# Kernel tuning notes

Measured on AMD Instinct MI355X. Metric: run time of the kernel, lower is better.

Reference implementation:

```python
import jax, jax.numpy as jnp
import numpy as np

E = 8
HIDDEN = 1024
INTER = 4096
CAPS = np.array([512, 1024, 2048, 4096, 1024, 512, 2048, 1024], dtype=np.int64)  # sum = 12288
TOTAL = int(CAPS.sum())


def setup_inputs() -> dict:
    key = jax.random.key(0)
    k1, k2, k3, k4, k5 = jax.random.split(key, 5)
    s1 = 1.0 / np.sqrt(HIDDEN)
    s2 = 1.0 / np.sqrt(INTER)
    return {
        "inter_state": jax.random.normal(k1, (TOTAL, HIDDEN), dtype=jnp.float32),
        "w1": jax.random.normal(k2, (E, INTER, HIDDEN), dtype=jnp.float32) * s1,
        "b1": jax.random.normal(k3, (E, INTER), dtype=jnp.float32) * s1,
        "w2": jax.random.normal(k4, (E, HIDDEN, INTER), dtype=jnp.float32) * s2,
        "b2": jax.random.normal(k5, (E, HIDDEN), dtype=jnp.float32) * s2,
        "capacities": jnp.asarray(CAPS),
    }


def reference(inter_state, w1, b1, w2, b2, capacities):
    # Grouped GEMM: tokens are contiguous per expert with sizes = capacities.
    # Capacities are routing metadata (static for slicing).
    caps = np.asarray(capacities)
    offs = np.concatenate([[0], np.cumsum(caps)]).astype(np.int64)
    outs = []
    for e in range(caps.shape[0]):  # small fixed expert loop
        x = inter_state[int(offs[e]):int(offs[e + 1])]      # [cap_e, hidden]
        h = x @ w1[e].T + b1[e]                              # [cap_e, inter]
        outs.append(h @ w2[e].T + b2[e])                     # [cap_e, hidden]
    return jnp.concatenate(outs, axis=0)                     # [total, hidden]
```

## Files before the change

kernel.cpp:

```cpp
#include <hip/hip_runtime.h>
#include <hip/hip_bf16.h>

#define DEV __device__ __forceinline__

typedef __bf16 bf16x8 __attribute__((ext_vector_type(8)));
typedef float  f32x4  __attribute__((ext_vector_type(4)));


DEV unsigned short f2bf(float f) {
  union { float f; unsigned u; } v; v.f = f;
  unsigned u = v.u;
  return (unsigned short)((u + 0x7FFFu + ((u >> 16) & 1u)) >> 16);
}

DEV float bf2f(unsigned short s) {
  union { unsigned u; float f; } v; v.u = (unsigned)s << 16; return v.f;
}

DEV void gld_lds16(const void* g, void* l) {
  __builtin_amdgcn_global_load_lds(
      (const __attribute__((address_space(1))) unsigned int*)g,
      (__attribute__((address_space(3))) unsigned int*)l, 16, 0, 0);
}

#define WAITVM(N) asm volatile("s_waitcnt vmcnt(" #N ")" ::: "memory"); \
                  __builtin_amdgcn_sched_barrier(0)
#define WAITLG(N) asm volatile("s_waitcnt lgkmcnt(" #N ")" ::: "memory"); \
                  __builtin_amdgcn_sched_barrier(0)
#define BARRIER() __builtin_amdgcn_s_barrier(); __builtin_amdgcn_sched_barrier(0)

template <int KT_, int KLEN, int SK, int N_, int NCT, bool OUT_BF16,
          bool HAS_BIAS, int EDIV>
__global__ __launch_bounds__(512, 2)
void gemm256p(const unsigned short* __restrict__ A,
              const unsigned short* __restrict__ B,
              const float* __restrict__ bias,
              void* __restrict__ C0, void* __restrict__ C1) {
  __shared__ __align__(128) char lds[131072];
  constexpr int NT = KLEN / 64;

  const int tid  = threadIdx.x;
  const int lane = tid & 63;
  const int wv   = tid >> 6;
  const int wm   = wv >> 2;
  const int wn   = wv & 3;
  const int fr   = lane & 15;
  const int fq   = lane >> 4;

  int bid = blockIdx.x;
  const int nwg = gridDim.x;
  bid = (bid & 7) * (nwg >> 3) + (bid >> 3);

  int sk = 0;
  if constexpr (SK > 1) {
    const int per = nwg / SK;
    sk = bid / per;
    bid -= sk * per;
  }
  const int kStart = sk * KLEN;
  void* Cv = (SK > 1 && sk == 1) ? C1 : C0;

  const int rt = bid / NCT;
  const int ct = bid - rt * NCT;

  int e;
  if constexpr (EDIV > 0) {
    e = rt / EDIV;
  } else {
    const int cums[9] = {0, 2, 6, 14, 30, 34, 36, 44, 48};
    e = 0;
#pragma unroll
    for (int i = 1; i < 8; ++i) e += (rt >= cums[i]) ? 1 : 0;
  }

  const int grow0 = rt * 256;
  const int nloc0 = ct * 256;
  const unsigned short* Bg = B + (size_t)e * N_ * KT_;

  f32x4 acc[8][4];
#pragma unroll
  for (int i = 0; i < 8; ++i)
#pragma unroll
    for (int j = 0; j < 4; ++j) acc[i][j] = (f32x4){0.f, 0.f, 0.f, 0.f};

  auto stage_half = [&](int t, int h) {
    const int kb = kStart + t * 64;
    char* dst = lds + (h >> 1) * 65536 + (t & 1) * 32768 + (h & 1) * 16384;
    const unsigned short* src = (h < 2) ? A : Bg;
    const int row0 = (h < 2) ? (grow0 + (h & 1) * 128) : (nloc0 + (h & 1) * 128);
#pragma unroll
    for (int s = 0; s < 2; ++s) {
      int o  = s * 8192 + wv * 1024 + lane * 16;
      int r  = o >> 7;
      int cb = (o & 127) ^ ((r & 7) << 4);
      gld_lds16(src + (size_t)(row0 + r) * KT_ + kb + (cb >> 1),
                dst + s * 8192 + wv * 1024);
    }
  };

  stage_half(0, 0); stage_half(0, 1); stage_half(0, 2); stage_half(0, 3);
  if constexpr (NT > 1) { stage_half(1, 2); stage_half(1, 3); }

  const int brow0 = (wn & 1) * 64;

  for (int t = 0; t < NT; ++t) {
    char* Ah = lds + (t & 1) * 32768 + wm * 16384;
    char* Bh = lds + 65536 + (t & 1) * 32768 + ((wn >> 1) * 16384);

    if (t + 1 < NT) { WAITVM(4); } else { WAITVM(0); }
    BARRIER();

    bf16x8 bfr[4][2], afX[2][2], afY[2][2];
#pragma unroll
    for (int ni = 0; ni < 4; ++ni) {
      int r = brow0 + ni * 16 + fr;
#pragma unroll
      for (int k = 0; k < 2; ++k)
        bfr[ni][k] = *(bf16x8*)(Bh + r * 128 + ((k * 64 + fq * 16) ^ ((r & 7) << 4)));
    }
#pragma unroll
    for (int j = 0; j < 2; ++j) {
      int r = j * 16 + fr;
#pragma unroll
      for (int k = 0; k < 2; ++k)
        afX[j][k] = *(bf16x8*)(Ah + r * 128 + ((k * 64 + fq * 16) ^ ((r & 7) << 4)));
    }
#pragma unroll
    for (int j = 0; j < 2; ++j) {
      int r = 32 + j * 16 + fr;
#pragma unroll
      for (int k = 0; k < 2; ++k)
        afY[j][k] = *(bf16x8*)(Ah + r * 128 + ((k * 64 + fq * 16) ^ ((r & 7) << 4)));
    }
    if (t + 1 < NT) stage_half(t + 1, 0);
    WAITLG(4);
    BARRIER();
    __builtin_amdgcn_s_setprio(1);
#pragma unroll
    for (int k = 0; k < 2; ++k)
#pragma unroll
      for (int j = 0; j < 2; ++j)
#pragma unroll
        for (int ni = 0; ni < 4; ++ni)
          acc[j][ni] = __builtin_amdgcn_mfma_f32_16x16x32_bf16(
              afX[j][k], bfr[ni][k], acc[j][ni], 0, 0, 0);
    __builtin_amdgcn_s_setprio(0);
#pragma unroll
    for (int j = 0; j < 2; ++j) {
      int r = 64 + j * 16 + fr;
#pragma unroll
      for (int k = 0; k < 2; ++k)
        afX[j][k] = *(bf16x8*)(Ah + r * 128 + ((k * 64 + fq * 16) ^ ((r & 7) << 4)));
    }
    if (t + 1 < NT) stage_half(t + 1, 1);
    if (t + 2 < NT) stage_half(t + 2, 2);
    WAITLG(4);
    __builtin_amdgcn_s_setprio(1);
#pragma unroll
    for (int k = 0; k < 2; ++k)
#pragma unroll
      for (int j = 0; j < 2; ++j)
#pragma unroll
        for (int ni = 0; ni < 4; ++ni)
          acc[2 + j][ni] = __builtin_amdgcn_mfma_f32_16x16x32_bf16(
              afY[j][k], bfr[ni][k], acc[2 + j][ni], 0, 0, 0);
    __builtin_amdgcn_s_setprio(0);
#pragma unroll
    for (int j = 0; j < 2; ++j) {
      int r = 96 + j * 16 + fr;
#pragma unroll
      for (int k = 0; k < 2; ++k)
        afY[j][k] = *(bf16x8*)(Ah + r * 128 + ((k * 64 + fq * 16) ^ ((r & 7) << 4)));
    }
    if (t + 2 < NT) stage_half(t + 2, 3);
    WAITLG(4);
    __builtin_amdgcn_s_setprio(1);
#pragma unroll
    for (int k = 0; k < 2; ++k)
#pragma unroll
      for (int j = 0; j < 2; ++j)
#pragma unroll
        for (int ni = 0; ni < 4; ++ni)
          acc[4 + j][ni] = __builtin_amdgcn_mfma_f32_16x16x32_bf16(
              afX[j][k], bfr[ni][k], acc[4 + j][ni], 0, 0, 0);
    __builtin_amdgcn_s_setprio(0);
    WAITLG(0);
    __builtin_amdgcn_s_setprio(1);
#pragma unroll
    for (int k = 0; k < 2; ++k)
#pragma unroll
      for (int j = 0; j < 2; ++j)
#pragma unroll
        for (int ni = 0; ni < 4; ++ni)
          acc[6 + j][ni] = __builtin_amdgcn_mfma_f32_16x16x32_bf16(
              afY[j][k], bfr[ni][k], acc[6 + j][ni], 0, 0, 0);
    __builtin_amdgcn_s_setprio(0);
  }

#pragma unroll
  for (int ni = 0; ni < 4; ++ni) {
    int ncol = nloc0 + wn * 64 + ni * 16 + fr;
    float bv = 0.f;
    if constexpr (HAS_BIAS) bv = (bias + (size_t)e * N_)[ncol];
#pragma unroll
    for (int mi = 0; mi < 8; ++mi) {
      int m = grow0 + wm * 128 + mi * 16 + fq * 4;
#pragma unroll
      for (int j = 0; j < 4; ++j) {
        float val = acc[mi][ni][j] + bv;
        if constexpr (OUT_BF16)
          ((unsigned short*)Cv)[(size_t)(m + j) * N_ + ncol] = f2bf(val);
        else
          ((float*)Cv)[(size_t)(m + j) * N_ + ncol] = val;
      }
    }
  }
}

template <int K_, int N_, int NCT, bool OUT_BF16, bool HAS_BIAS, int EDIV>
__global__ __launch_bounds__(256, 2)
void gemm128(const unsigned short* __restrict__ A,
             const unsigned short* __restrict__ B,
             const float* __restrict__ bias, void* __restrict__ Cv) {
  __shared__ __align__(128) char lds[2][32768];
  constexpr int NT = K_ / 64;

  const int tid  = threadIdx.x;
  const int lane = tid & 63;
  const int wv   = tid >> 6;
  const int wm   = wv >> 1;
  const int wn   = wv & 1;
  const int fr   = lane & 15;
  const int fq   = lane >> 4;

  int bid = blockIdx.x;
  const int nwg = gridDim.x;
  bid = (bid & 7) * (nwg >> 3) + (bid >> 3);

  const int rt = bid / NCT;
  const int ct = bid - rt * NCT;

  int e;
  if constexpr (EDIV > 0) {
    e = rt / EDIV;
  } else {
    const int cums[9] = {0, 4, 12, 28, 60, 68, 72, 88, 96};
    e = 0;
#pragma unroll
    for (int i = 1; i < 8; ++i) e += (rt >= cums[i]) ? 1 : 0;
  }

  const int grow0 = rt * 128;
  const int nloc0 = ct * 128;
  const unsigned short* Bg = B + (size_t)e * N_ * K_;

  f32x4 acc[4][4];
#pragma unroll
  for (int i = 0; i < 4; ++i)
#pragma unroll
    for (int j = 0; j < 4; ++j) acc[i][j] = (f32x4){0.f, 0.f, 0.f, 0.f};

  auto stage = [&](int buf, int tk) {
    const int kb = tk * 64;
#pragma unroll
    for (int s = 0; s < 4; ++s) {
      int o  = s * 4096 + wv * 1024 + lane * 16;
      int r  = o >> 7;
      int cb = (o & 127) ^ ((r & 7) << 4);
      gld_lds16(A + (size_t)(grow0 + r) * K_ + kb + (cb >> 1),
                lds[buf] + s * 4096 + wv * 1024);
    }
#pragma unroll
    for (int s = 0; s < 4; ++s) {
      int o  = s * 4096 + wv * 1024 + lane * 16;
      int r  = o >> 7;
      int cb = (o & 127) ^ ((r & 7) << 4);
      gld_lds16(Bg + (size_t)(nloc0 + r) * K_ + kb + (cb >> 1),
                lds[buf] + 16384 + s * 4096 + wv * 1024);
    }
  };

  stage(0, 0);
  for (int t = 0; t < NT; ++t) {
    const int cur = t & 1;
    if (t + 1 < NT) {
      stage(cur ^ 1, t + 1);
      WAITVM(8);
    } else {
      WAITVM(0);
    }
    BARRIER();

    char* Ab = lds[cur];
    char* Bb = lds[cur] + 16384;
    bf16x8 af[4][2], bf[4][2];
#pragma unroll
    for (int mi = 0; mi < 4; ++mi) {
      int r = wm * 64 + mi * 16 + fr;
#pragma unroll
      for (int k = 0; k < 2; ++k)
        af[mi][k] = *(bf16x8*)(Ab + r * 128 + ((k * 64 + fq * 16) ^ ((r & 7) << 4)));
    }
#pragma unroll
    for (int ni = 0; ni < 4; ++ni) {
      int r = wn * 64 + ni * 16 + fr;
#pragma unroll
      for (int k = 0; k < 2; ++k)
        bf[ni][k] = *(bf16x8*)(Bb + r * 128 + ((k * 64 + fq * 16) ^ ((r & 7) << 4)));
    }
    WAITLG(0);
    __builtin_amdgcn_s_setprio(1);
#pragma unroll
    for (int k = 0; k < 2; ++k)
#pragma unroll
      for (int mi = 0; mi < 4; ++mi)
#pragma unroll
        for (int ni = 0; ni < 4; ++ni)
          acc[mi][ni] = __builtin_amdgcn_mfma_f32_16x16x32_bf16(
              af[mi][k], bf[ni][k], acc[mi][ni], 0, 0, 0);
    __builtin_amdgcn_s_setprio(0);
    BARRIER();
  }

#pragma unroll
  for (int ni = 0; ni < 4; ++ni) {
    int ncol = nloc0 + wn * 64 + ni * 16 + fr;
    float bv = 0.f;
    if constexpr (HAS_BIAS) bv = (bias + (size_t)e * N_)[ncol];
#pragma unroll
    for (int mi = 0; mi < 4; ++mi) {
      int m = grow0 + wm * 64 + mi * 16 + fq * 4;
#pragma unroll
      for (int j = 0; j < 4; ++j) {
        float val = acc[mi][ni][j] + bv;
        if constexpr (OUT_BF16)
          ((unsigned short*)Cv)[(size_t)(m + j) * N_ + ncol] = f2bf(val);
        else
          ((float*)Cv)[(size_t)(m + j) * N_ + ncol] = val;
      }
    }
  }
}

__global__ __launch_bounds__(256)
void reduce_bf16(const unsigned short* __restrict__ p0,
                 const unsigned short* __restrict__ p1,
                 unsigned short* __restrict__ out, int n8) {
  for (int i = blockIdx.x * 256 + threadIdx.x; i < n8; i += gridDim.x * 256) {
    ushort4 a0 = ((const ushort4*)p0)[2 * i];
    ushort4 a1 = ((const ushort4*)p0)[2 * i + 1];
    ushort4 b0 = ((const ushort4*)p1)[2 * i];
    ushort4 b1 = ((const ushort4*)p1)[2 * i + 1];
    ushort4 r0 = {f2bf(bf2f(a0.x) + bf2f(b0.x)), f2bf(bf2f(a0.y) + bf2f(b0.y)),
                  f2bf(bf2f(a0.z) + bf2f(b0.z)), f2bf(bf2f(a0.w) + bf2f(b0.w))};
    ushort4 r1 = {f2bf(bf2f(a1.x) + bf2f(b1.x)), f2bf(bf2f(a1.y) + bf2f(b1.y)),
                  f2bf(bf2f(a1.z) + bf2f(b1.z)), f2bf(bf2f(a1.w) + bf2f(b1.w))};
    ((ushort4*)out)[2 * i]     = r0;
    ((ushort4*)out)[2 * i + 1] = r1;
  }
}

DEV int swz(int r, int cbyte) {
  return (r * 64 + cbyte) ^ (((r >> 1) & 7) << 4);
}

template <int K_, int N_, bool OUT_BF16, bool HAS_BIAS, int EDIV>
__global__ __launch_bounds__(512, 2)
void gemm8(const unsigned short* __restrict__ A,
           const unsigned short* __restrict__ B,
           const float* __restrict__ bias, void* __restrict__ Cv) {
  __shared__ __align__(128) char lds[2][49152];
  const int t    = threadIdx.x;
  const int lane = t & 63;
  const int wv   = t >> 6;
  const int wm   = wv >> 1;
  const int wn   = wv & 1;
  const int fr   = lane & 15;
  const int fq   = lane >> 4;
  constexpr int NCT = N_ / 128;
  constexpr int NT  = K_ / 64;

  int bid = blockIdx.x;
  const int nwg = gridDim.x;
  bid = (bid & 7) * (nwg >> 3) + (bid >> 3);
  const int rt = bid / NCT;
  const int ct = bid - rt * NCT;

  int e;
  if constexpr (EDIV > 0) {
    e = rt / EDIV;
  } else {
    const int cums[9] = {0, 2, 6, 14, 30, 34, 36, 44, 48};
    e = 0;
#pragma unroll
    for (int i = 1; i < 8; ++i) e += (rt >= cums[i]) ? 1 : 0;
  }

  const int grow0 = rt * 256;
  const int nloc0 = ct * 128;
  const unsigned short* Bg = B + (size_t)e * N_ * K_;

  f32x4 acc[4][4];
#pragma unroll
  for (int i = 0; i < 4; ++i)
#pragma unroll
    for (int j = 0; j < 4; ++j) acc[i][j] = (f32x4){0.f, 0.f, 0.f, 0.f};

  auto stage = [&](int buf, int tk) {
    const int kb = tk * 64;
    char* Abase = lds[buf];
    char* Bbase = lds[buf] + 32768;
#pragma unroll
    for (int s = 0; s < 4; ++s) {
      int o  = s * 8192 + wv * 1024 + lane * 16;
      int r  = o >> 7;
      int cb = (o & 127) ^ ((r & 7) << 4);
      gld_lds16(A + (size_t)(grow0 + r) * K_ + kb + (cb >> 1),
                Abase + s * 8192 + wv * 1024);
    }
#pragma unroll
    for (int s = 0; s < 2; ++s) {
      int o  = s * 8192 + wv * 1024 + lane * 16;
      int r  = o >> 7;
      int cb = (o & 127) ^ ((r & 7) << 4);
      gld_lds16(Bg + (size_t)(nloc0 + r) * K_ + kb + (cb >> 1),
                Bbase + s * 8192 + wv * 1024);
    }
  };

  auto compute = [&](int buf) {
    char* Abase = lds[buf];
    char* Bbase = lds[buf] + 32768;
    bf16x8 af[4][2], bf[4][2];
#pragma unroll
    for (int mi = 0; mi < 4; ++mi) {
      int r = wm * 64 + mi * 16 + fr;
#pragma unroll
      for (int k = 0; k < 2; ++k)
        af[mi][k] = *(bf16x8*)(Abase + r * 128 + ((k * 64 + fq * 16) ^ ((r & 7) << 4)));
    }
#pragma unroll
    for (int ni = 0; ni < 4; ++ni) {
      int r = wn * 64 + ni * 16 + fr;
#pragma unroll
      for (int k = 0; k < 2; ++k)
        bf[ni][k] = *(bf16x8*)(Bbase + r * 128 + ((k * 64 + fq * 16) ^ ((r & 7) << 4)));
    }
    __builtin_amdgcn_s_setprio(1);
#pragma unroll
    for (int k = 0; k < 2; ++k)
#pragma unroll
      for (int mi = 0; mi < 4; ++mi)
#pragma unroll
        for (int ni = 0; ni < 4; ++ni)
          acc[mi][ni] = __builtin_amdgcn_mfma_f32_16x16x32_bf16(
              af[mi][k], bf[ni][k], acc[mi][ni], 0, 0, 0);
    __builtin_amdgcn_s_setprio(0);
  };

  stage(0, 0);
  for (int tk = 0; tk < NT; ++tk) {
    const int cur = tk & 1;
    if (tk + 1 < NT) {
      stage(cur ^ 1, tk + 1);
      WAITVM(6);
    } else {
      WAITVM(0);
    }
    __builtin_amdgcn_s_barrier();
    compute(cur);
    WAITLG(0);
    __builtin_amdgcn_s_barrier();
  }

#pragma unroll
  for (int ni = 0; ni < 4; ++ni) {
    int nloc = nloc0 + wn * 64 + ni * 16 + fr;
    float bv = 0.f;
    if constexpr (HAS_BIAS) bv = (bias + (size_t)e * N_)[nloc];
#pragma unroll
    for (int mi = 0; mi < 4; ++mi) {
      int m = grow0 + wm * 64 + mi * 16 + fq * 4;
#pragma unroll
      for (int j = 0; j < 4; ++j) {
        float val = acc[mi][ni][j] + bv;
        if constexpr (OUT_BF16)
          ((unsigned short*)Cv)[(size_t)(m + j) * N_ + nloc] = f2bf(val);
        else
          ((float*)Cv)[(size_t)(m + j) * N_ + nloc] = val;
      }
    }
  }
}

template <int K_, int N_, int NCT_, bool OUT_BF16, bool HAS_BIAS, int EDIV>
__global__ __launch_bounds__(256)
void gemm_expert(const void* __restrict__ Av, const void* __restrict__ Bv,
                 const float* __restrict__ bias, void* __restrict__ Cv) {
  __shared__ char lds[2][12288];
  const int t    = threadIdx.x;
  const int lane = t & 63;
  const int wv   = t >> 6;
  const int wr   = wv >> 1;
  const int wc   = wv & 1;
  const int fr   = lane & 15;
  const int fq   = lane >> 4;

  int bid = blockIdx.x;
  const int nwg = gridDim.x;
  if ((nwg & 7) == 0) bid = (bid & 7) * (nwg >> 3) + (bid >> 3);
  const int rt = bid / NCT_;
  const int ct = bid - rt * NCT_;

  int e;
  if constexpr (EDIV > 0) {
    e = rt / EDIV;
  } else {
    const int cums[9] = {0, 4, 12, 28, 60, 68, 72, 88, 96};
    e = 0;
#pragma unroll
    for (int i = 1; i < 8; ++i) e += (rt >= cums[i]) ? 1 : 0;
  }

  const int grow0 = rt * 128;
  const int nloc0 = ct * 64;

  f32x4 acc[4][2];
#pragma unroll
  for (int i = 0; i < 4; ++i)
#pragma unroll
    for (int j = 0; j < 2; ++j) acc[i][j] = (f32x4){0.f, 0.f, 0.f, 0.f};

  const float* Af = (const float*)Av;
  const unsigned short* Bb = (const unsigned short*)Bv + (size_t)e * N_ * K_;

  auto stage = [&](int buf, int kb) {
    char* As = lds[buf];
    char* Bs = lds[buf] + 8192;
#pragma unroll
    for (int it = 0; it < 4; ++it) {
      int q = t + it * 256, r = q >> 3, c = (q & 7) * 4;
      float4 f = *(const float4*)(Af + (size_t)(grow0 + r) * K_ + kb + c);
      ushort4 v = {f2bf(f.x), f2bf(f.y), f2bf(f.z), f2bf(f.w)};
      *(ushort4*)(As + swz(r, c * 2)) = v;
    }
    int o = wv * 1024 + lane * 16;
    int p = o ^ (((o >> 7) & 7) << 4);
    gld_lds16(Bb + (size_t)(nloc0 + (p >> 6)) * K_ + kb + ((p & 63) >> 1),
              Bs + wv * 1024);
  };

  auto compute = [&](int buf) {
    char* As = lds[buf];
    char* Bs = lds[buf] + 8192;
    bf16x8 af[4], bfg[2];
#pragma unroll
    for (int mi = 0; mi < 4; ++mi)
      af[mi] = *(bf16x8*)(As + swz(wr * 64 + mi * 16 + fr, fq * 16));
#pragma unroll
    for (int ni = 0; ni < 2; ++ni)
      bfg[ni] = *(bf16x8*)(Bs + swz(wc * 32 + ni * 16 + fr, fq * 16));
#pragma unroll
    for (int mi = 0; mi < 4; ++mi)
#pragma unroll
      for (int ni = 0; ni < 2; ++ni)
        acc[mi][ni] = __builtin_amdgcn_mfma_f32_16x16x32_bf16(
            af[mi], bfg[ni], acc[mi][ni], 0, 0, 0);
  };

  int cur = 0;
  stage(0, 0);
  __syncthreads();
  for (int kb = 32; kb < K_; kb += 32) {
    stage(cur ^ 1, kb);
    compute(cur);
    __syncthreads();
    cur ^= 1;
  }
  compute(cur);

#pragma unroll
  for (int ni = 0; ni < 2; ++ni) {
    int nloc = nloc0 + wc * 32 + ni * 16 + fr;
    float bv = 0.f;
    if constexpr (HAS_BIAS) bv = (bias + (size_t)e * N_)[nloc];
#pragma unroll
    for (int mi = 0; mi < 4; ++mi) {
      int m = grow0 + wr * 64 + mi * 16 + fq * 4;
#pragma unroll
      for (int j = 0; j < 4; ++j) {
        float val = acc[mi][ni][j] + bv;
        if constexpr (OUT_BF16)
          ((unsigned short*)Cv)[(size_t)(m + j) * N_ + nloc] = f2bf(val);
        else
          ((float*)Cv)[(size_t)(m + j) * N_ + nloc] = val;
      }
    }
  }
}

__global__ __launch_bounds__(256)
void transpose_w1(const float* __restrict__ w1, unsigned short* __restrict__ w1t) {
  __shared__ unsigned short tl[64 * 68];
  int b = blockIdx.x;
  int jt = b & 15, kt = (b >> 4) & 63, e = b >> 10;
  const float* src = w1 + ((size_t)e * 4096 + kt * 64) * 1024 + jt * 64;
  int t = threadIdx.x;
#pragma unroll
  for (int it = 0; it < 4; ++it) {
    int q = t + it * 256, kr = q >> 4, jc = (q & 15) * 4;
    float4 f = *(const float4*)(src + (size_t)kr * 1024 + jc);
    ushort4 v = {f2bf(f.x), f2bf(f.y), f2bf(f.z), f2bf(f.w)};
    *(ushort4*)&tl[kr * 68 + jc] = v;
  }
  __syncthreads();
  unsigned short* dst = w1t + ((size_t)e * 1024 + jt * 64) * 4096 + kt * 64;
#pragma unroll
  for (int it = 0; it < 4; ++it) {
    int q = t + it * 256, jr = q >> 4, kc = (q & 15) * 4;
    ushort4 v = {tl[(kc + 0) * 68 + jr], tl[(kc + 1) * 68 + jr],
                 tl[(kc + 2) * 68 + jr], tl[(kc + 3) * 68 + jr]};
    *(ushort4*)(dst + (size_t)jr * 4096 + kc) = v;
  }
}

template <bool STORE_BF>
__global__ __launch_bounds__(256)
void conv_w2_bias(const float* __restrict__ w2, const float* __restrict__ b1,
                  const float* __restrict__ b2, unsigned short* __restrict__ w2bf,
                  float* __restrict__ bc) {
  int row = blockIdx.x, e = row >> 10, t = threadIdx.x;
  const float* src = w2 + (size_t)row * 4096;
  const float* b1e = b1 + (size_t)e * 4096;
  float acc = 0.f;
#pragma unroll
  for (int it = 0; it < 4; ++it) {
    int c = (t + it * 256) * 4;
    float4 f = *(const float4*)(src + c);
    float4 g = *(const float4*)(b1e + c);
    acc += f.x * g.x + f.y * g.y + f.z * g.z + f.w * g.w;
    if constexpr (STORE_BF) {
      ushort4 v = {f2bf(f.x), f2bf(f.y), f2bf(f.z), f2bf(f.w)};
      *(ushort4*)(w2bf + (size_t)row * 4096 + c) = v;
    }
  }
#pragma unroll
  for (int o = 32; o > 0; o >>= 1) acc += __shfl_down(acc, o);
  __shared__ float red[4];
  if ((t & 63) == 0) red[t >> 6] = acc;
  __syncthreads();
  if (t == 0) bc[row] = red[0] + red[1] + red[2] + red[3] + b2[row];
}

__global__ __launch_bounds__(256)
void conv_f32_bf16(const float* __restrict__ in, unsigned short* __restrict__ out,
                   int n4) {
  for (int i = blockIdx.x * 256 + threadIdx.x; i < n4; i += gridDim.x * 256) {
    float4 f = *(const float4*)(in + (size_t)i * 4);
    ushort4 v = {f2bf(f.x), f2bf(f.y), f2bf(f.z), f2bf(f.w)};
    *(ushort4*)(out + (size_t)i * 4) = v;
  }
}

extern "C" void kernel_launch(void* const* d_in, const int* in_sizes, int n_in,
                              void* d_out, int out_size, void* d_ws, size_t ws_size,
                              hipStream_t stream) {
  const float* x  = (const float*)d_in[0];
  const float* w1 = (const float*)d_in[1];
  const float* b1 = (const float*)d_in[2];
  const float* w2 = (const float*)d_in[3];
  const float* b2 = (const float*)d_in[4];

  char* ws = (char*)d_ws;
  unsigned short* w1t = (unsigned short*)ws;
  const size_t NEED_T2 = 151126016, NEED_T3 = 176291840;

  if (ws_size >= NEED_T3) {
    unsigned short* w2bf = (unsigned short*)(ws + 67108864);
    unsigned short* Wc   = (unsigned short*)(ws + 134217728);
    float*          bc   = (float*)(ws + 150994944);
    unsigned short* xbf  = (unsigned short*)(ws + 151126016);
    unsigned short* p1   = xbf;

    transpose_w1<<<8192, 256, 0, stream>>>(w1, w1t);
    conv_w2_bias<true><<<8192, 256, 0, stream>>>(w2, b1, b2, w2bf, bc);
    gemm256p<4096, 2048, 2, 1024, 4, true, false, 4>
        <<<256, 512, 0, stream>>>(w2bf, w1t, nullptr, Wc, p1);
    reduce_bf16<<<2048, 256, 0, stream>>>(Wc, p1, Wc, 8 * 1024 * 1024 / 8);
    conv_f32_bf16<<<2048, 256, 0, stream>>>(x, xbf, 12288 * 1024 / 4);
    gemm128<1024, 1024, 8, false, true, 0>
        <<<768, 256, 0, stream>>>(xbf, Wc, bc, (float*)d_out);
  } else if (ws_size >= NEED_T2) {
    unsigned short* w2bf = (unsigned short*)(ws + 67108864);
    unsigned short* Wc   = (unsigned short*)(ws + 134217728);
    float*          bc   = (float*)(ws + 150994944);

    transpose_w1<<<8192, 256, 0, stream>>>(w1, w1t);
    conv_w2_bias<true><<<8192, 256, 0, stream>>>(w2, b1, b2, w2bf, bc);
    gemm8<4096, 1024, true, false, 4>
        <<<256, 512, 0, stream>>>(w2bf, w1t, nullptr, Wc);
    gemm_expert<1024, 1024, 16, false, true, 0>
        <<<1536, 256, 0, stream>>>(x, Wc, bc, d_out);
  } else {
    unsigned short* Wc = (unsigned short*)(ws + 67108864);
    float*          bc = (float*)(ws + 83886080);

    transpose_w1<<<8192, 256, 0, stream>>>(w1, w1t);
    conv_w2_bias<false><<<8192, 256, 0, stream>>>(w2, b1, b2, nullptr, bc);
    gemm_expert<4096, 1024, 8, true, false, 8>
        <<<768, 256, 0, stream>>>(w2, w1t, nullptr, Wc);
    gemm_expert<1024, 1024, 16, false, true, 0>
        <<<1536, 256, 0, stream>>>(x, Wc, bc, d_out);
  }
}
```

Before: 201.0 us.

## Fuse split-K reduction and x bf16 conversion into final expert GEMM

Drops the separate reduce_bf16 and conv_f32_bf16 launches. The final 128x128 GEMM now loads fp32 x and the two bf16 split-K partials directly into registers, converts and sums them, and writes the results to LDS. Global loads for the next K tile are issued before the MFMAs on the current tile to hide their latency. This saves two launches and their global round trips, but replaces the async global_load_lds path with register staging, and the combined weight is re-reduced by every row tile that reads it.

Measured after the change: 230.9 us. +14.9%, slower.

```diff
diff --git a/kernel.cpp b/kernel.cpp
--- a/kernel.cpp
+++ b/kernel.cpp
@@ -217,13 +217,13 @@
   }
 }
 
-template <int K_, int N_, int NCT, bool OUT_BF16, bool HAS_BIAS, int EDIV>
 __global__ __launch_bounds__(256, 2)
-void gemm128(const unsigned short* __restrict__ A,
-             const unsigned short* __restrict__ B,
-             const float* __restrict__ bias, void* __restrict__ Cv) {
+void gemm128rs(const float* __restrict__ X,
+               const unsigned short* __restrict__ P0,
+               const unsigned short* __restrict__ P1,
+               const float* __restrict__ bias, float* __restrict__ C) {
+  constexpr int K_ = 1024, N_ = 1024, NCT = 8, NT = K_ / 64;
   __shared__ __align__(128) char lds[2][32768];
-  constexpr int NT = K_ / 64;
 
   const int tid  = threadIdx.x;
   const int lane = tid & 63;
@@ -240,19 +240,16 @@
   const int rt = bid / NCT;
   const int ct = bid - rt * NCT;
 
-  int e;
-  if constexpr (EDIV > 0) {
-    e = rt / EDIV;
-  } else {
-    const int cums[9] = {0, 4, 12, 28, 60, 68, 72, 88, 96};
-    e = 0;
-#pragma unroll
-    for (int i = 1; i < 8; ++i) e += (rt >= cums[i]) ? 1 : 0;
-  }
+  const int cums[9] = {0, 4, 12, 28, 60, 68, 72, 88, 96};
+  int e = 0;
+#pragma unroll
+  for (int i = 1; i < 8; ++i) e += (rt >= cums[i]) ? 1 : 0;
 
   const int grow0 = rt * 128;
   const int nloc0 = ct * 128;
-  const unsigned short* Bg = B + (size_t)e * N_ * K_;
+  const float*          Xb  = X  + (size_t)grow0 * K_;
+  const unsigned short* P0b = P0 + ((size_t)e * 1024 + nloc0) * K_;
+  const unsigned short* P1b = P1 + ((size_t)e * 1024 + nloc0) * K_;
 
   f32x4 acc[4][4];
 #pragma unroll
@@ -260,39 +257,50 @@
 #pragma unroll
     for (int j = 0; j < 4; ++j) acc[i][j] = (f32x4){0.f, 0.f, 0.f, 0.f};
 
-  auto stage = [&](int buf, int tk) {
-    const int kb = tk * 64;
-#pragma unroll
-    for (int s = 0; s < 4; ++s) {
-      int o  = s * 4096 + wv * 1024 + lane * 16;
-      int r  = o >> 7;
-      int cb = (o & 127) ^ ((r & 7) << 4);
-      gld_lds16(A + (size_t)(grow0 + r) * K_ + kb + (cb >> 1),
-                lds[buf] + s * 4096 + wv * 1024);
-    }
-#pragma unroll
-    for (int s = 0; s < 4; ++s) {
-      int o  = s * 4096 + wv * 1024 + lane * 16;
-      int r  = o >> 7;
-      int cb = (o & 127) ^ ((r & 7) << 4);
-      gld_lds16(Bg + (size_t)(nloc0 + r) * K_ + kb + (cb >> 1),
-                lds[buf] + 16384 + s * 4096 + wv * 1024);
+  const int rA = tid >> 4;
+  const int cA = (tid & 15) * 4;
+
+  float4  aR[8];
+  ushort4 b0R[8], b1R[8];
+
+  auto load_regs = [&](int t) {
+    const int kb = t * 64;
+#pragma unroll
+    for (int s = 0; s < 8; ++s) {
+      int r = rA + s * 16;
+      aR[s]  = *(const float4*)(Xb + (size_t)r * K_ + kb + cA);
+      b0R[s] = *(const ushort4*)(P0b + (size_t)r * K_ + kb + cA);
+      b1R[s] = *(const ushort4*)(P1b + (size_t)r * K_ + kb + cA);
     }
   };
 
-  stage(0, 0);
+  auto write_lds = [&](int t) {
+    char* As = lds[t & 1];
+    char* Bs = lds[t & 1] + 16384;
+#pragma unroll
+    for (int s = 0; s < 8; ++s) {
+      int r  = rA + s * 16;
+      int cb = (cA * 2) ^ ((r & 7) << 4);
+      ushort4 va = {f2bf(aR[s].x), f2bf(aR[s].y), f2bf(aR[s].z), f2bf(aR[s].w)};
+      *(ushort4*)(As + r * 128 + cb) = va;
+      ushort4 vb = {f2bf(bf2f(b0R[s].x) + bf2f(b1R[s].x)),
+                    f2bf(bf2f(b0R[s].y) + bf2f(b1R[s].y)),
+                    f2bf(bf2f(b0R[s].z) + bf2f(b1R[s].z)),
+                    f2bf(bf2f(b0R[s].w) + bf2f(b1R[s].w))};
+      *(ushort4*)(Bs + r * 128 + cb) = vb;
+    }
+  };
+
+  load_regs(0);
+  WAITVM(0);
+  write_lds(0);
+  BARRIER();
+
   for (int t = 0; t < NT; ++t) {
-    const int cur = t & 1;
-    if (t + 1 < NT) {
-      stage(cur ^ 1, t + 1);
-      WAITVM(8);
-    } else {
-      WAITVM(0);
-    }
-    BARRIER();
-
-    char* Ab = lds[cur];
-    char* Bb = lds[cur] + 16384;
+    if (t + 1 < NT) load_regs(t + 1);
+
+    char* Ab = lds[t & 1];
+    char* Bb = lds[t & 1] + 16384;
     bf16x8 af[4][2], bf[4][2];
 #pragma unroll
     for (int mi = 0; mi < 4; ++mi) {
@@ -319,44 +327,25 @@
           acc[mi][ni] = __builtin_amdgcn_mfma_f32_16x16x32_bf16(
               af[mi][k], bf[ni][k], acc[mi][ni], 0, 0, 0);
     __builtin_amdgcn_s_setprio(0);
+
+    if (t + 1 < NT) {
+      WAITVM(0);
+      write_lds(t + 1);
+    }
     BARRIER();
   }
 
 #pragma unroll
   for (int ni = 0; ni < 4; ++ni) {
     int ncol = nloc0 + wn * 64 + ni * 16 + fr;
-    float bv = 0.f;
-    if constexpr (HAS_BIAS) bv = (bias + (size_t)e * N_)[ncol];
+    float bv = (bias + (size_t)e * N_)[ncol];
 #pragma unroll
     for (int mi = 0; mi < 4; ++mi) {
       int m = grow0 + wm * 64 + mi * 16 + fq * 4;
 #pragma unroll
-      for (int j = 0; j < 4; ++j) {
-        float val = acc[mi][ni][j] + bv;
-        if constexpr (OUT_BF16)
-          ((unsigned short*)Cv)[(size_t)(m + j) * N_ + ncol] = f2bf(val);
-        else
-          ((float*)Cv)[(size_t)(m + j) * N_ + ncol] = val;
-      }
-    }
-  }
-}
-
-__global__ __launch_bounds__(256)
-void reduce_bf16(const unsigned short* __restrict__ p0,
-                 const unsigned short* __restrict__ p1,
-                 unsigned short* __restrict__ out, int n8) {
-  for (int i = blockIdx.x * 256 + threadIdx.x; i < n8; i += gridDim.x * 256) {
-    ushort4 a0 = ((const ushort4*)p0)[2 * i];
-    ushort4 a1 = ((const ushort4*)p0)[2 * i + 1];
-    ushort4 b0 = ((const ushort4*)p1)[2 * i];
-    ushort4 b1 = ((const ushort4*)p1)[2 * i + 1];
-    ushort4 r0 = {f2bf(bf2f(a0.x) + bf2f(b0.x)), f2bf(bf2f(a0.y) + bf2f(b0.y)),
-                  f2bf(bf2f(a0.z) + bf2f(b0.z)), f2bf(bf2f(a0.w) + bf2f(b0.w))};
-    ushort4 r1 = {f2bf(bf2f(a1.x) + bf2f(b1.x)), f2bf(bf2f(a1.y) + bf2f(b1.y)),
-                  f2bf(bf2f(a1.z) + bf2f(b1.z)), f2bf(bf2f(a1.w) + bf2f(b1.w))};
-    ((ushort4*)out)[2 * i]     = r0;
-    ((ushort4*)out)[2 * i + 1] = r1;
+      for (int j = 0; j < 4; ++j)
+        C[(size_t)(m + j) * N_ + ncol] = acc[mi][ni][j] + bv;
+    }
   }
 }
 
@@ -652,16 +641,6 @@
   if (t == 0) bc[row] = red[0] + red[1] + red[2] + red[3] + b2[row];
 }
 
-__global__ __launch_bounds__(256)
-void conv_f32_bf16(const float* __restrict__ in, unsigned short* __restrict__ out,
-                   int n4) {
-  for (int i = blockIdx.x * 256 + threadIdx.x; i < n4; i += gridDim.x * 256) {
-    float4 f = *(const float4*)(in + (size_t)i * 4);
-    ushort4 v = {f2bf(f.x), f2bf(f.y), f2bf(f.z), f2bf(f.w)};
-    *(ushort4*)(out + (size_t)i * 4) = v;
-  }
-}
-
 extern "C" void kernel_launch(void* const* d_in, const int* in_sizes, int n_in,
                               void* d_out, int out_size, void* d_ws, size_t ws_size,
                               hipStream_t stream) {
@@ -673,23 +652,19 @@
 
   char* ws = (char*)d_ws;
   unsigned short* w1t = (unsigned short*)ws;
-  const size_t NEED_T2 = 151126016, NEED_T3 = 176291840;
+  const size_t NEED_T2 = 151126016, NEED_T3 = 167903232;
 
   if (ws_size >= NEED_T3) {
     unsigned short* w2bf = (unsigned short*)(ws + 67108864);
-    unsigned short* Wc   = (unsigned short*)(ws + 134217728);
+    unsigned short* p0   = (unsigned short*)(ws + 134217728);
     float*          bc   = (float*)(ws + 150994944);
-    unsigned short* xbf  = (unsigned short*)(ws + 151126016);
-    unsigned short* p1   = xbf;
+    unsigned short* p1   = (unsigned short*)(ws + 151126016);
 
     transpose_w1<<<8192, 256, 0, stream>>>(w1, w1t);
     conv_w2_bias<true><<<8192, 256, 0, stream>>>(w2, b1, b2, w2bf, bc);
     gemm256p<4096, 2048, 2, 1024, 4, true, false, 4>
-        <<<256, 512, 0, stream>>>(w2bf, w1t, nullptr, Wc, p1);
-    reduce_bf16<<<2048, 256, 0, stream>>>(Wc, p1, Wc, 8 * 1024 * 1024 / 8);
-    conv_f32_bf16<<<2048, 256, 0, stream>>>(x, xbf, 12288 * 1024 / 4);
-    gemm128<1024, 1024, 8, false, true, 0>
-        <<<768, 256, 0, stream>>>(xbf, Wc, bc, (float*)d_out);
+        <<<256, 512, 0, stream>>>(w2bf, w1t, nullptr, p0, p1);
+    gemm128rs<<<768, 256, 0, stream>>>(x, p0, p1, bc, (float*)d_out);
   } else if (ws_size >= NEED_T2) {
     unsigned short* w2bf = (unsigned short*)(ws + 67108864);
     unsigned short* Wc   = (unsigned short*)(ws + 134217728);
```
